# Kernel optimization log

Hardware: AMD Instinct MI355X
Metric: run time of the kernel (lower is better)

## Reference

```python
import jax, jax.numpy as jnp
import numpy as np

CLASS_EMBED_DIM = 128
TOPK = 64
EPS = float(np.finfo(float).eps)
ALPHA = 0.99


def setup_inputs() -> dict:
    key = jax.random.key(0)
    k1, k2, k3 = jax.random.split(key, 3)
    b, n, d = 16, 256, 640  # d = embed_dim + class_embed_dim
    embed_dim, inner_dim = 512, 512
    x = jax.random.normal(k1, (b, n, d), dtype=jnp.float32)
    # kaiming-normal style init: std = sqrt(2 / fan_in)
    std = (2.0 / embed_dim) ** 0.5
    Wq = jax.random.normal(k2, (embed_dim, inner_dim), dtype=jnp.float32) * std
    Wk = jax.random.normal(k3, (embed_dim, inner_dim), dtype=jnp.float32) * std
    alpha = jnp.float32(ALPHA)
    return {"x": x, "Wq": Wq, "Wk": Wk, "alpha": alpha}


def reference(x, Wq, Wk, alpha):
    b, n, d = x.shape
    xf = x.reshape(b * n, d)            # (N, embed+class)
    xe = xf[:, :-CLASS_EMBED_DIM]       # (N, embed)
    q = xe @ Wq                         # (N, inner)
    k = xe @ Wk                         # (N, inner)
    D = q.shape[1]
    # dots[i,j] = mean_d (q_i - k_j)^2, via expansion (avoids N x N x D tensor)
    q2 = jnp.sum(q * q, axis=1)
    k2 = jnp.sum(k * k, axis=1)
    dots = (q2[:, None] + k2[None, :] - 2.0 * (q @ k.T)) / D  # (N, N)
    N = dots.shape[0]
    _, idx = jax.lax.top_k(dots, TOPK)  # largest, matching torch.topk
    mask = jnp.zeros_like(dots).at[jnp.arange(N)[:, None], idx].set(1.0)
    mask = ((mask + mask.T) > 0).astype(jnp.float32)
    attn = dots * mask
    A = jnp.eye(N, dtype=dots.dtype) - alpha * attn + EPS
    out = jnp.linalg.inv(A) @ xf        # (N, d); to_v is identity
    return out.reshape(b, n, d)
```

## Files before the change

kernel.cpp:

```cpp
#include <hip/hip_runtime.h>
#include <float.h>

#define NN 4096
#define DD 640
#define DE 512
#define NB 16
#define OB 128
#define NOB (NN/OB)
#define SB 128
#define NSB (NN/SB)

static __device__ __forceinline__ float4 ldg4(const float* p) { return *(const float4*)p; }

__global__ __launch_bounds__(256) void proj_gemm(
    const float* __restrict__ xf, const float* __restrict__ Wq,
    const float* __restrict__ Wk, float* __restrict__ q, float* __restrict__ kk_)
{
  __shared__ float Xs[32][68], Qs[32][68], Ks[32][68];
  const int i0 = blockIdx.x * 64, c0 = blockIdx.y * 64;
  const int t = threadIdx.x, tr = t >> 4, tc = t & 15;
  float accq[4][4] = {}, acck[4][4] = {};
  for (int kb = 0; kb < DE; kb += 32) {
    {
      int m = t >> 3, k4 = (t & 7) << 2;
      float4 v0 = ldg4(xf + (size_t)(i0 + m) * DD + kb + k4);
      float4 v1 = ldg4(xf + (size_t)(i0 + m + 32) * DD + kb + k4);
      Xs[k4+0][m] = v0.x; Xs[k4+1][m] = v0.y; Xs[k4+2][m] = v0.z; Xs[k4+3][m] = v0.w;
      Xs[k4+0][m+32] = v1.x; Xs[k4+1][m+32] = v1.y; Xs[k4+2][m+32] = v1.z; Xs[k4+3][m+32] = v1.w;
    }
    {
      int kr = t >> 3, n8 = (t & 7) << 3;
      *(float4*)&Qs[kr][n8]   = ldg4(Wq + (size_t)(kb + kr) * DE + c0 + n8);
      *(float4*)&Qs[kr][n8+4] = ldg4(Wq + (size_t)(kb + kr) * DE + c0 + n8 + 4);
      *(float4*)&Ks[kr][n8]   = ldg4(Wk + (size_t)(kb + kr) * DE + c0 + n8);
      *(float4*)&Ks[kr][n8+4] = ldg4(Wk + (size_t)(kb + kr) * DE + c0 + n8 + 4);
    }
    __syncthreads();
    #pragma unroll
    for (int kkk = 0; kkk < 32; ++kkk) {
      float a[4], bq[4], bk[4];
      *(float4*)a  = *(const float4*)&Xs[kkk][tr << 2];
      *(float4*)bq = *(const float4*)&Qs[kkk][tc << 2];
      *(float4*)bk = *(const float4*)&Ks[kkk][tc << 2];
      #pragma unroll
      for (int r = 0; r < 4; ++r)
        #pragma unroll
        for (int c = 0; c < 4; ++c) { accq[r][c] += a[r]*bq[c]; acck[r][c] += a[r]*bk[c]; }
    }
    __syncthreads();
  }
  #pragma unroll
  for (int r = 0; r < 4; ++r) {
    float* qp = q   + (size_t)(i0 + (tr<<2) + r) * DE + c0 + (tc<<2);
    float* kp = kk_ + (size_t)(i0 + (tr<<2) + r) * DE + c0 + (tc<<2);
    *(float4*)qp = make_float4(accq[r][0], accq[r][1], accq[r][2], accq[r][3]);
    *(float4*)kp = make_float4(acck[r][0], acck[r][1], acck[r][2], acck[r][3]);
  }
}

__global__ __launch_bounds__(256) void rownorm(
    const float* __restrict__ q, const float* __restrict__ kk_,
    float* __restrict__ q2, float* __restrict__ k2)
{
  int w = (blockIdx.x * 256 + threadIdx.x) >> 6;
  int lane = threadIdx.x & 63;
  const float* src = (w < NN) ? q : kk_;
  int row = (w < NN) ? w : w - NN;
  const float* p = src + (size_t)row * DE;
  float s = 0.f;
  for (int c = lane; c < DE; c += 64) { float v = p[c]; s += v * v; }
  for (int off = 32; off; off >>= 1) s += __shfl_down(s, off);
  if (lane == 0) { if (w < NN) q2[row] = s; else k2[row] = s; }
}

__global__ __launch_bounds__(256) void dots_gemm(
    const float* __restrict__ q, const float* __restrict__ kk_,
    const float* __restrict__ q2, const float* __restrict__ k2,
    float* __restrict__ dots)
{
  __shared__ float Qs[32][68], Ks[32][68];
  const int i0 = blockIdx.x * 64, j0 = blockIdx.y * 64;
  const int t = threadIdx.x, tr = t >> 4, tc = t & 15;
  float acc[4][4] = {};
  for (int kb = 0; kb < DE; kb += 32) {
    int m = t >> 3, k4 = (t & 7) << 2;
    {
      float4 v0 = ldg4(q + (size_t)(i0 + m) * DE + kb + k4);
      float4 v1 = ldg4(q + (size_t)(i0 + m + 32) * DE + kb + k4);
      Qs[k4+0][m] = v0.x; Qs[k4+1][m] = v0.y; Qs[k4+2][m] = v0.z; Qs[k4+3][m] = v0.w;
      Qs[k4+0][m+32] = v1.x; Qs[k4+1][m+32] = v1.y; Qs[k4+2][m+32] = v1.z; Qs[k4+3][m+32] = v1.w;
    }
    {
      float4 v0 = ldg4(kk_ + (size_t)(j0 + m) * DE + kb + k4);
      float4 v1 = ldg4(kk_ + (size_t)(j0 + m + 32) * DE + kb + k4);
      Ks[k4+0][m] = v0.x; Ks[k4+1][m] = v0.y; Ks[k4+2][m] = v0.z; Ks[k4+3][m] = v0.w;
      Ks[k4+0][m+32] = v1.x; Ks[k4+1][m+32] = v1.y; Ks[k4+2][m+32] = v1.z; Ks[k4+3][m+32] = v1.w;
    }
    __syncthreads();
    #pragma unroll
    for (int kkk = 0; kkk < 32; ++kkk) {
      float a[4], b[4];
      *(float4*)a = *(const float4*)&Qs[kkk][tr << 2];
      *(float4*)b = *(const float4*)&Ks[kkk][tc << 2];
      #pragma unroll
      for (int r = 0; r < 4; ++r)
        #pragma unroll
        for (int c = 0; c < 4; ++c) acc[r][c] += a[r]*b[c];
    }
    __syncthreads();
  }
  const float inv = 1.0f / (float)DE;
  float k2v[4]; *(float4*)k2v = ldg4(k2 + j0 + (tc<<2));
  #pragma unroll
  for (int r = 0; r < 4; ++r) {
    float q2v = q2[i0 + (tr<<2) + r];
    float o[4];
    #pragma unroll
    for (int c = 0; c < 4; ++c) o[c] = (q2v + k2v[c] - 2.0f*acc[r][c]) * inv;
    *(float4*)(dots + (size_t)(i0 + (tr<<2) + r) * NN + j0 + (tc<<2)) =
        make_float4(o[0], o[1], o[2], o[3]);
  }
}

__global__ __launch_bounds__(256) void topk_bits(
    const float* __restrict__ dots, unsigned int* __restrict__ bits)
{
  __shared__ float row[NN];
  __shared__ unsigned int b[128];
  __shared__ float rv[4]; __shared__ int ri[4];
  const int i = blockIdx.x, t = threadIdx.x;
  const float* dr = dots + (size_t)i * NN;
  for (int c = t; c < NN; c += 256) row[c] = dr[c];
  if (t < 128) b[t] = 0u;
  __syncthreads();
  for (int it = 0; it < 64; ++it) {
    float bv = -FLT_MAX; int bi = NN;
    for (int c = t; c < NN; c += 256) { float v = row[c]; if (v > bv) { bv = v; bi = c; } }
    for (int off = 32; off; off >>= 1) {
      float ov = __shfl_down(bv, off); int oi = __shfl_down(bi, off);
      if (ov > bv || (ov == bv && oi < bi)) { bv = ov; bi = oi; }
    }
    if ((t & 63) == 0) { rv[t >> 6] = bv; ri[t >> 6] = bi; }
    __syncthreads();
    if (t == 0) {
      float fv = rv[0]; int fi = ri[0];
      for (int w = 1; w < 4; ++w)
        if (rv[w] > fv || (rv[w] == fv && ri[w] < fi)) { fv = rv[w]; fi = ri[w]; }
      b[fi >> 5] |= 1u << (fi & 31);
      row[fi] = -FLT_MAX;
    }
    __syncthreads();
  }
  if (t < 128) bits[(size_t)i * 128 + t] = b[t];
}

__global__ __launch_bounds__(256) void build_A(
    float* __restrict__ A, const unsigned int* __restrict__ bits,
    const float* __restrict__ alpha_p)
{
  int tid = blockIdx.x * 256 + threadIdx.x;
  int i = tid >> 10;
  int j4 = (tid & 1023) << 2;
  float alpha = alpha_p[0];
  float* p = A + (size_t)i * NN + j4;
  float4 d = *(float4*)p;
  unsigned int wrow = bits[(size_t)i * 128 + (j4 >> 5)];
  float dv[4] = {d.x, d.y, d.z, d.w}, o[4];
  #pragma unroll
  for (int u = 0; u < 4; ++u) {
    int j = j4 + u;
    unsigned int m1 = (wrow >> (j & 31)) & 1u;
    unsigned int m2 = (bits[(size_t)j * 128 + (i >> 5)] >> (i & 31)) & 1u;
    float base = (i == j) ? 1.0f : 0.0f;
    o[u] = base - ((m1 | m2) ? alpha * dv[u] : 0.0f);
  }
  *(float4*)p = make_float4(o[0], o[1], o[2], o[3]);
}

__global__ __launch_bounds__(1024) void lu_panel(
    float* __restrict__ A, int k0, int ok0, int* __restrict__ piv)
{
  const int t = threadIdx.x;
  const int M = NN - k0;
  float a[4][NB];
  __shared__ float bufA[NB], bufB[NB];
  __shared__ float rv[16]; __shared__ int ri[16];
  __shared__ int s_pr;
  __shared__ int piv_s[NB];
  __shared__ int sd[32], ss[32];
  __shared__ float l16[16][17];
  __shared__ float gbuf[32][112];

  #pragma unroll
  for (int i = 0; i < 4; ++i) {
    int r = t + (i << 10);
    if (r < M) {
      const float* src = A + (size_t)(k0 + r) * NN + k0;
      #pragma unroll
      for (int c4 = 0; c4 < NB; c4 += 4) {
        float4 v = ldg4(src + c4);
        a[i][c4] = v.x; a[i][c4+1] = v.y; a[i][c4+2] = v.z; a[i][c4+3] = v.w;
      }
    }
  }

  #pragma unroll
  for (int j = 0; j < NB; ++j) {
    float bv = -1.0f; int br = 1 << 30;
    #pragma unroll
    for (int i = 0; i < 4; ++i) {
      int r = t + (i << 10);
      if (r >= j && r < M) {
        float v = fabsf(a[i][j]);
        if (v > bv || (v == bv && r < br)) { bv = v; br = r; }
      }
    }
    for (int off = 32; off; off >>= 1) {
      float ov = __shfl_down(bv, off); int orr = __shfl_down(br, off);
      if (ov > bv || (ov == bv && orr < br)) { bv = ov; br = orr; }
    }
    if ((t & 63) == 0) { rv[t >> 6] = bv; ri[t >> 6] = br; }
    __syncthreads();
    if (t == 0) {
      float fv = rv[0]; int fr = ri[0];
      for (int w = 1; w < 16; ++w)
        if (rv[w] > fv || (rv[w] == fv && ri[w] < fr)) { fv = rv[w]; fr = ri[w]; }
      s_pr = fr; piv_s[j] = k0 + fr;
    }
    __syncthreads();
    const int pr = s_pr, prT = pr & 1023, prS = pr >> 10;
    if (t == prT) {
      #pragma unroll
      for (int i2 = 0; i2 < 4; ++i2) if (i2 == prS) {
        #pragma unroll
        for (int c = 0; c < NB; ++c) bufB[c] = a[i2][c];
      }
    }
    if (t == j) {
      #pragma unroll
      for (int c = 0; c < NB; ++c) bufA[c] = a[0][c];
    }
    __syncthreads();
    if (t == j) {
      #pragma unroll
      for (int c = 0; c < NB; ++c) a[0][c] = bufB[c];
    }
    if (t == prT) {
      #pragma unroll
      for (int i2 = 0; i2 < 4; ++i2) if (i2 == prS) {
        #pragma unroll
        for (int c = 0; c < NB; ++c) a[i2][c] = bufA[c];
      }
    }
    float rp = 1.0f / bufB[j];
    #pragma unroll
    for (int i = 0; i < 4; ++i) {
      int r = t + (i << 10);
      if (r > j && r < M) {
        float mlt = a[i][j] * rp;
        a[i][j] = mlt;
        #pragma unroll
        for (int c = j + 1; c < NB; ++c) a[i][c] -= mlt * bufB[c];
      }
    }
    __syncthreads();
  }

  #pragma unroll
  for (int i = 0; i < 4; ++i) {
    int r = t + (i << 10);
    if (r < M) {
      float* dst = A + (size_t)(k0 + r) * NN + k0;
      #pragma unroll
      for (int c4 = 0; c4 < NB; c4 += 4)
        *(float4*)(dst + c4) = make_float4(a[i][c4], a[i][c4+1], a[i][c4+2], a[i][c4+3]);
    }
  }
  if (t < NB) piv[k0 + t] = piv_s[t];

  if (t < 16) {
    #pragma unroll
    for (int c2 = 0; c2 < NB; ++c2) l16[t][c2] = a[0][c2];
  }

  if (t < 32) {
    int slotrow = (t < NB) ? (k0 + t) : -1;
    int content = slotrow;
    int next_ext = NB;
    for (int j = 0; j < NB; ++j) {
      int p = piv_s[j];
      unsigned long long mask = __ballot(slotrow == p);
      int bslot;
      if (mask) bslot = __ffsll((unsigned long long)mask) - 1;
      else {
        bslot = next_ext;
        if (t == next_ext) { slotrow = p; content = p; }
        next_ext++;
      }
      int srcl = (t == j) ? bslot : ((t == bslot) ? j : t);
      content = __shfl(content, srcl);
    }
    sd[t] = slotrow;
    ss[t] = content;
  }
  __syncthreads();

  const int p16 = k0 - ok0;
  for (int idx = t; idx < 32 * 112; idx += 1024) {
    int i = idx / 112, cc = idx - i * 112;
    if (sd[i] >= 0 && sd[i] != ss[i]) {
      int c = ok0 + (cc < p16 ? cc : cc + NB);
      gbuf[i][cc] = A[(size_t)ss[i] * NN + c];
    }
  }
  __syncthreads();
  for (int idx = t; idx < 32 * 112; idx += 1024) {
    int i = idx / 112, cc = idx - i * 112;
    if (sd[i] >= 0 && sd[i] != ss[i]) {
      int c = ok0 + (cc < p16 ? cc : cc + NB);
      A[(size_t)sd[i] * NN + c] = gbuf[i][cc];
    }
  }
  __syncthreads();

  const int w = ok0 + OB - (k0 + NB);
  if (t < w) {
    int c = k0 + NB + t;
    int cc = p16 + t;
    float x[16];
    #pragma unroll
    for (int i = 0; i < 16; ++i)
      x[i] = (ss[i] != sd[i]) ? gbuf[i][cc] : A[(size_t)(k0 + i) * NN + c];
    #pragma unroll
    for (int i = 1; i < 16; ++i)
      #pragma unroll
      for (int j = 0; j < i; ++j) x[i] -= l16[i][j] * x[j];
    #pragma unroll
    for (int i = 0; i < 16; ++i) A[(size_t)(k0 + i) * NN + c] = x[i];
  }
}

__global__ __launch_bounds__(128) void net_perm128(
    const int* __restrict__ piv_g, int ok0,
    int* __restrict__ nd, int* __restrict__ ns)
{
  __shared__ int slotrow[256], content[256];
  __shared__ int found, next_ext;
  const int t = threadIdx.x;
  slotrow[t] = ok0 + t;       content[t] = ok0 + t;
  slotrow[t + 128] = -1;      content[t + 128] = -1;
  if (t == 0) next_ext = 128;
  for (int j = 0; j < OB; ++j) {
    __syncthreads();
    int p = piv_g[ok0 + j];
    if (t == 0) found = (p < ok0 + OB) ? (p - ok0) : -1;
    __syncthreads();
    if (p >= ok0 + OB && slotrow[t + 128] == p) found = t + 128;
    __syncthreads();
    if (t == 0) {
      int s2 = found;
      if (s2 < 0) { s2 = next_ext++; slotrow[s2] = p; content[s2] = p; }
      int tmp = content[j]; content[j] = content[s2]; content[s2] = tmp;
    }
  }
  __syncthreads();
  nd[t] = slotrow[t];           ns[t] = content[t];
  nd[t + 128] = slotrow[t + 128]; ns[t + 128] = content[t + 128];
}

__global__ __launch_bounds__(256) void perm_copy_out(
    const float* __restrict__ A, float* __restrict__ T,
    const int* __restrict__ nd, const int* __restrict__ ns, int ok0)
{
  int s = blockIdx.y;
  int d = nd[s], sr = ns[s];
  if (d < 0 || d == sr) return;
  int c = blockIdx.x * 1024 + threadIdx.x * 4;
  if (c >= ok0 && c < ok0 + OB) return;
  *(float4*)(T + (size_t)s * NN + c) = ldg4(A + (size_t)sr * NN + c);
}

__global__ __launch_bounds__(256) void perm_copy_in(
    float* __restrict__ A, const float* __restrict__ T,
    const int* __restrict__ nd, const int* __restrict__ ns, int ok0)
{
  int s = blockIdx.y;
  int d = nd[s], sr = ns[s];
  if (d < 0 || d == sr) return;
  int c = blockIdx.x * 1024 + threadIdx.x * 4;
  if (c >= ok0 && c < ok0 + OB) return;
  *(float4*)(A + (size_t)d * NN + c) = ldg4(T + (size_t)s * NN + c);
}

__global__ __launch_bounds__(64) void trsm128L(float* __restrict__ A, int ok0)
{
  __shared__ float Ls[64][65];
  __shared__ float xs[64][132];
  const int t = threadIdx.x;
  const int c = ok0 + OB + blockIdx.x * 64 + t;
  for (int i = 0; i < 128; ++i) xs[t][i] = A[(size_t)(ok0 + i) * NN + c];
  for (int i = 0; i < 64; ++i) Ls[i][t] = A[(size_t)(ok0 + i) * NN + ok0 + t];
  __syncthreads();
  for (int i = 1; i < 64; ++i) {
    float s = 0.f;
    #pragma unroll 4
    for (int j = 0; j < i; ++j) s += Ls[i][j] * xs[t][j];
    xs[t][i] -= s;
  }
  __syncthreads();
  for (int i = 0; i < 64; ++i) Ls[i][t] = A[(size_t)(ok0 + 64 + i) * NN + ok0 + t];
  __syncthreads();
  for (int i = 0; i < 64; ++i) {
    float s = 0.f;
    #pragma unroll 4
    for (int j = 0; j < 64; ++j) s += Ls[i][j] * xs[t][j];
    xs[t][64 + i] -= s;
  }
  __syncthreads();
  for (int i = 0; i < 64; ++i) Ls[i][t] = A[(size_t)(ok0 + 64 + i) * NN + ok0 + 64 + t];
  __syncthreads();
  for (int i = 1; i < 64; ++i) {
    float s = 0.f;
    #pragma unroll 4
    for (int j = 0; j < i; ++j) s += Ls[i][j] * xs[t][64 + j];
    xs[t][64 + i] -= s;
  }
  for (int i = 0; i < 128; ++i) A[(size_t)(ok0 + i) * NN + c] = xs[t][i];
}

__global__ __launch_bounds__(256) void rank_update(
    float* __restrict__ C, int ldc,
    const float* __restrict__ Aop, int lda,
    const float* __restrict__ Bop, int ldb,
    int Mr, int Nc, int K)
{
  __shared__ float As[16][68], Bs[16][68];
  const int m0 = blockIdx.x * 64, n0 = blockIdx.y * 64;
  const int t = threadIdx.x, tr = t >> 4, tc = t & 15;
  const float4 z4 = make_float4(0.f, 0.f, 0.f, 0.f);
  float acc[4][4] = {};
  for (int kb = 0; kb < K; kb += 16) {
    {
      int m = t >> 2, k4 = (t & 3) << 2;
      float4 v0 = (m0 + m < Mr) ? ldg4(Aop + (size_t)(m0 + m) * lda + kb + k4) : z4;
      As[k4+0][m] = v0.x; As[k4+1][m] = v0.y; As[k4+2][m] = v0.z; As[k4+3][m] = v0.w;
    }
    {
      int kr = t >> 4, n4 = (t & 15) << 2;
      bool ok = (n0 + n4 < Nc);
      float4 w0 = ok ? ldg4(Bop + (size_t)(kb + kr) * ldb + n0 + n4) : z4;
      *(float4*)&Bs[kr][n4] = w0;
    }
    __syncthreads();
    #pragma unroll
    for (int kkk = 0; kkk < 16; ++kkk) {
      float a[4], b[4];
      *(float4*)a = *(const float4*)&As[kkk][tr << 2];
      *(float4*)b = *(const float4*)&Bs[kkk][tc << 2];
      #pragma unroll
      for (int r = 0; r < 4; ++r)
        #pragma unroll
        for (int c = 0; c < 4; ++c) acc[r][c] += a[r] * b[c];
    }
    __syncthreads();
  }
  #pragma unroll
  for (int r = 0; r < 4; ++r) {
    int m = m0 + (tr << 2) + r;
    int n = n0 + (tc << 2);
    if (m < Mr && n < Nc) {
      float* cp = C + (size_t)m * ldc + n;
      float4 cv = *(float4*)cp;
      cv.x -= acc[r][0]; cv.y -= acc[r][1]; cv.z -= acc[r][2]; cv.w -= acc[r][3];
      *(float4*)cp = cv;
    }
  }
}

__global__ __launch_bounds__(128) void inv_tri(
    const float* __restrict__ Ag, float* __restrict__ invT, int upper)
{
  __shared__ float xs[128][128];
  const int s = blockIdx.x, t = threadIdx.x;
  const size_t r0 = (size_t)s * SB;
  for (int i = 0; i < 128; ++i) xs[i][t] = 0.0f;
  const float* Tb = Ag + r0 * NN + r0;
  if (!upper) {
    xs[t][t] = 1.0f;
    for (int i = 1; i < 128; ++i) {
      float ssum = 0.f;
      for (int j = 0; j < i; ++j) ssum += Tb[(size_t)i * NN + j] * xs[j][t];
      if (i != t) xs[i][t] = -ssum;
    }
  } else {
    xs[t][t] = 1.0f / Tb[(size_t)t * NN + t];
    for (int i = 126; i >= 0; --i) {
      float ssum = 0.f;
      for (int j = i + 1; j < 128; ++j) ssum += Tb[(size_t)i * NN + j] * xs[j][t];
      if (i != t) xs[i][t] = -ssum / Tb[(size_t)i * NN + i];
    }
  }
  for (int i = 0; i < 128; ++i) invT[(size_t)s * SB * SB + (size_t)i * SB + t] = xs[i][t];
}

__global__ __launch_bounds__(1024) void perm_compose(
    const int* __restrict__ piv, int* __restrict__ idxp)
{
  __shared__ int pl[NN];
  const int t = threadIdx.x;
  for (int j = t; j < NN; j += 1024) pl[j] = piv[j];
  __syncthreads();
  int pos[4] = { t, t + 1024, t + 2048, t + 3072 };
  for (int j = NN - 1; j >= 0; --j) {
    int p = pl[j];
    #pragma unroll
    for (int u = 0; u < 4; ++u) {
      int r = t + (u << 10);
      if (j <= r) {
        if (pos[u] == j) pos[u] = p;
        else if (pos[u] == p) pos[u] = j;
      }
    }
  }
  #pragma unroll
  for (int u = 0; u < 4; ++u) idxp[t + (u << 10)] = pos[u];
}

__global__ __launch_bounds__(256) void gather_rows(
    const float* __restrict__ xf, const int* __restrict__ idxp, float* __restrict__ out)
{
  const int r = blockIdx.x, t = threadIdx.x;
  const int src = idxp[r];
  const float4* s = (const float4*)(xf + (size_t)src * DD);
  float4* d = (float4*)(out + (size_t)r * DD);
  for (int c = t; c < DD / 4; c += 256) d[c] = s[c];
}

__global__ __launch_bounds__(256) void diag_apply(
    float* __restrict__ B, const float* __restrict__ Minv, int r0)
{
  __shared__ float Bs[128][68];
  const int c0 = blockIdx.x * 64, t = threadIdx.x;
  #pragma unroll
  for (int v = 0; v < 8; ++v) {
    int id = t + v * 256;
    int k = id >> 4, c4 = (id & 15) << 2;
    *(float4*)&Bs[k][c4] = ldg4(B + (size_t)(r0 + k) * DD + c0 + c4);
  }
  __syncthreads();
  const int tr = t >> 4, tc = t & 15;
  float acc[8][4] = {};
  for (int k4 = 0; k4 < 128; k4 += 4) {
    float b0[4], b1[4], b2[4], b3[4];
    *(float4*)b0 = *(const float4*)&Bs[k4+0][tc << 2];
    *(float4*)b1 = *(const float4*)&Bs[k4+1][tc << 2];
    *(float4*)b2 = *(const float4*)&Bs[k4+2][tc << 2];
    *(float4*)b3 = *(const float4*)&Bs[k4+3][tc << 2];
    #pragma unroll
    for (int rr = 0; rr < 8; ++rr) {
      float m[4]; *(float4*)m = ldg4(Minv + (size_t)(tr*8 + rr) * SB + k4);
      #pragma unroll
      for (int c = 0; c < 4; ++c)
        acc[rr][c] += m[0]*b0[c] + m[1]*b1[c] + m[2]*b2[c] + m[3]*b3[c];
    }
  }
  #pragma unroll
  for (int rr = 0; rr < 8; ++rr)
    *(float4*)(B + (size_t)(r0 + tr*8 + rr) * DD + c0 + (tc << 2)) =
        make_float4(acc[rr][0], acc[rr][1], acc[rr][2], acc[rr][3]);
}

extern "C" void kernel_launch(void* const* d_in, const int* in_sizes, int n_in,
                              void* d_out, int out_size, void* d_ws, size_t ws_size,
                              hipStream_t stream)
{
  const float* xf    = (const float*)d_in[0];
  const float* Wq    = (const float*)d_in[1];
  const float* Wk    = (const float*)d_in[2];
  const float* alpha = (const float*)d_in[3];
  float* out = (float*)d_out;
  char* ws = (char*)d_ws;

  float* Amat = (float*)(ws);
  float* q    = (float*)(ws + 67108864ull);
  float* kbuf = (float*)(ws + 75497472ull);
  float* invL = (float*)(ws + 83886080ull);
  float* invU = (float*)(ws + 85983232ull);
  unsigned int* bits = (unsigned int*)(ws + 88080384ull);
  float* q2   = (float*)(ws + 90177536ull);
  float* k2   = (float*)(ws + 90193920ull);
  int* piv    = (int*)(ws + 90210304ull);
  int* idxp   = (int*)(ws + 90226688ull);
  int* nd     = (int*)(ws + 90243072ull);
  int* ns     = (int*)(ws + 90275840ull);
  float* Tbuf = q;

  proj_gemm<<<dim3(NN/64, DE/64), 256, 0, stream>>>(xf, Wq, Wk, q, kbuf);
  rownorm<<<2 * NN / 4, 256, 0, stream>>>(q, kbuf, q2, k2);
  dots_gemm<<<dim3(NN/64, NN/64), 256, 0, stream>>>(q, kbuf, q2, k2, Amat);
  topk_bits<<<NN, 256, 0, stream>>>(Amat, bits);
  build_A<<<NN * NN / 4 / 256, 256, 0, stream>>>(Amat, bits, alpha);

  for (int ob = 0; ob < NOB; ++ob) {
    const int ok0 = ob * OB;
    for (int p = 0; p < OB / NB; ++p) {
      const int k0 = ok0 + p * NB;
      lu_panel<<<1, 1024, 0, stream>>>(Amat, k0, ok0, piv);
      if (p < OB / NB - 1) {
        const int k1 = k0 + NB;
        const int w = ok0 + OB - k1;
        const int M2 = NN - k1;
        rank_update<<<dim3((M2 + 63) / 64, (w + 63) / 64), 256, 0, stream>>>(
            Amat + (size_t)k1 * NN + k1, NN,
            Amat + (size_t)k1 * NN + k0, NN,
            Amat + (size_t)k0 * NN + k1, NN,
            M2, w, NB);
      }
    }
    net_perm128<<<1, 128, 0, stream>>>(piv, ok0, nd, ns);
    perm_copy_out<<<dim3(NN / 1024, 256), 256, 0, stream>>>(Amat, Tbuf, nd, ns, ok0);
    perm_copy_in<<<dim3(NN / 1024, 256), 256, 0, stream>>>(Amat, Tbuf, nd, ns, ok0);
    const int b1 = ok0 + OB;
    const int M2 = NN - b1;
    if (M2 > 0) {
      trsm128L<<<M2 / 64, 64, 0, stream>>>(Amat, ok0);
      rank_update<<<dim3(M2 / 64, M2 / 64), 256, 0, stream>>>(
          Amat + (size_t)b1 * NN + b1, NN,
          Amat + (size_t)b1 * NN + ok0, NN,
          Amat + (size_t)ok0 * NN + b1, NN,
          M2, M2, OB);
    }
  }

  inv_tri<<<NSB, 128, 0, stream>>>(Amat, invL, 0);
  inv_tri<<<NSB, 128, 0, stream>>>(Amat, invU, 1);
  perm_compose<<<1, 1024, 0, stream>>>(piv, idxp);
  gather_rows<<<NN, 256, 0, stream>>>(xf, idxp, out);

  for (int s = 0; s < NSB; ++s) {
    int r0 = s * SB;
    diag_apply<<<DD / 64, 256, 0, stream>>>(out, invL + (size_t)s * SB * SB, r0);
    if (r0 + SB < NN) {
      int M2 = NN - r0 - SB;
      rank_update<<<dim3(M2 / 64, DD / 64), 256, 0, stream>>>(
          out + (size_t)(r0 + SB) * DD, DD,
          Amat + (size_t)(r0 + SB) * NN + r0, NN,
          out + (size_t)r0 * DD, DD,
          M2, DD, SB);
    }
  }
  for (int s = NSB - 1; s >= 0; --s) {
    int r0 = s * SB;
    diag_apply<<<DD / 64, 256, 0, stream>>>(out, invU + (size_t)s * SB * SB, r0);
    if (r0 > 0) {
      rank_update<<<dim3(r0 / 64, DD / 64), 256, 0, stream>>>(
          out, DD,
          Amat + r0, NN,
          out + (size_t)r0 * DD, DD,
          r0, DD, SB);
    }
  }
}
```

Measured before the change: 40.80 ms.

## Use 128x128 register-tiled trailing update, warp-level pivot permutation, split accumulators

Adds a rank_update128 kernel with 8x8 per-thread register tiles over 128x128 output tiles. It replaces the 64x64 kernel for the big trailing LU update and for both block triangular solves, raising arithmetic intensity. net_perm128 is rewritten as a single-wavefront kernel that uses ballot and shuffle instead of shared memory and repeated barriers. The trsm and triangular-inverse dot loops get four independent accumulators to break the FMA dependency chain, which also changes summation order slightly. The larger tiles mean fewer blocks on the small late-stage updates, and DD/128=5 assumes exact divisibility.

```diff
diff --git a/kernel.cpp b/kernel.cpp
--- a/kernel.cpp
+++ b/kernel.cpp
@@ -340,32 +340,50 @@
   }
 }
 
-__global__ __launch_bounds__(128) void net_perm128(
+__global__ __launch_bounds__(64) void net_perm128(
     const int* __restrict__ piv_g, int ok0,
     int* __restrict__ nd, int* __restrict__ ns)
 {
-  __shared__ int slotrow[256], content[256];
-  __shared__ int found, next_ext;
-  const int t = threadIdx.x;
-  slotrow[t] = ok0 + t;       content[t] = ok0 + t;
-  slotrow[t + 128] = -1;      content[t + 128] = -1;
-  if (t == 0) next_ext = 128;
+  __shared__ int pl[OB];
+  const int L = threadIdx.x;
+  pl[L] = piv_g[ok0 + L];
+  pl[L + 64] = piv_g[ok0 + 64 + L];
+  __syncthreads();
+  int c0 = ok0 + L, c1 = ok0 + 64 + L, c2 = -1, c3 = -1;
+  int sr2 = -1, sr3 = -1;
+  int next_ext = 128;
   for (int j = 0; j < OB; ++j) {
-    __syncthreads();
-    int p = piv_g[ok0 + j];
-    if (t == 0) found = (p < ok0 + OB) ? (p - ok0) : -1;
-    __syncthreads();
-    if (p >= ok0 + OB && slotrow[t + 128] == p) found = t + 128;
-    __syncthreads();
-    if (t == 0) {
-      int s2 = found;
-      if (s2 < 0) { s2 = next_ext++; slotrow[s2] = p; content[s2] = p; }
-      int tmp = content[j]; content[j] = content[s2]; content[s2] = tmp;
-    }
-  }
-  __syncthreads();
-  nd[t] = slotrow[t];           ns[t] = content[t];
-  nd[t + 128] = slotrow[t + 128]; ns[t + 128] = content[t + 128];
+    int p = pl[j];
+    int s2;
+    if (p < ok0 + OB) s2 = p - ok0;
+    else {
+      unsigned long long m2 = __ballot(sr2 == p);
+      unsigned long long m3 = __ballot(sr3 == p);
+      if (m2) s2 = 128 + (__ffsll(m2) - 1);
+      else if (m3) s2 = 192 + (__ffsll(m3) - 1);
+      else {
+        s2 = next_ext;
+        if (s2 < 192) { if (L == s2 - 128) { sr2 = p; c2 = p; } }
+        else          { if (L == s2 - 192) { sr3 = p; c3 = p; } }
+        next_ext++;
+      }
+    }
+    int jp = j >> 6, jl = j & 63, sp = s2 >> 6, sl = s2 & 63;
+    int vj0 = __shfl(c0, jl), vj1 = __shfl(c1, jl);
+    int vj = (jp == 0) ? vj0 : vj1;
+    int vs0 = __shfl(c0, sl), vs1 = __shfl(c1, sl), vs2 = __shfl(c2, sl), vs3 = __shfl(c3, sl);
+    int vs = (sp == 0) ? vs0 : (sp == 1) ? vs1 : (sp == 2) ? vs2 : vs3;
+    if (jp == 0 && L == jl) c0 = vs;
+    if (jp == 1 && L == jl) c1 = vs;
+    if (sp == 0 && L == sl) c0 = vj;
+    if (sp == 1 && L == sl) c1 = vj;
+    if (sp == 2 && L == sl) c2 = vj;
+    if (sp == 3 && L == sl) c3 = vj;
+  }
+  nd[L] = ok0 + L;        ns[L] = c0;
+  nd[64 + L] = ok0 + 64 + L; ns[64 + L] = c1;
+  nd[128 + L] = sr2;      ns[128 + L] = c2;
+  nd[192 + L] = sr3;      ns[192 + L] = c3;
 }
 
 __global__ __launch_bounds__(256) void perm_copy_out(
@@ -395,35 +413,46 @@
 __global__ __launch_bounds__(64) void trsm128L(float* __restrict__ A, int ok0)
 {
   __shared__ float Ls[64][65];
-  __shared__ float xs[64][132];
+  __shared__ float xs[64][133];
   const int t = threadIdx.x;
   const int c = ok0 + OB + blockIdx.x * 64 + t;
   for (int i = 0; i < 128; ++i) xs[t][i] = A[(size_t)(ok0 + i) * NN + c];
   for (int i = 0; i < 64; ++i) Ls[i][t] = A[(size_t)(ok0 + i) * NN + ok0 + t];
   __syncthreads();
   for (int i = 1; i < 64; ++i) {
-    float s = 0.f;
+    float s0 = 0.f, s1 = 0.f, s2 = 0.f, s3 = 0.f;
+    int j = 0;
+    for (; j + 3 < i; j += 4) {
+      s0 += Ls[i][j+0] * xs[t][j+0]; s1 += Ls[i][j+1] * xs[t][j+1];
+      s2 += Ls[i][j+2] * xs[t][j+2]; s3 += Ls[i][j+3] * xs[t][j+3];
+    }
+    for (; j < i; ++j) s0 += Ls[i][j] * xs[t][j];
+    xs[t][i] -= (s0 + s1) + (s2 + s3);
+  }
+  __syncthreads();
+  for (int i = 0; i < 64; ++i) Ls[i][t] = A[(size_t)(ok0 + 64 + i) * NN + ok0 + t];
+  __syncthreads();
+  for (int i = 0; i < 64; ++i) {
+    float s0 = 0.f, s1 = 0.f, s2 = 0.f, s3 = 0.f;
     #pragma unroll 4
-    for (int j = 0; j < i; ++j) s += Ls[i][j] * xs[t][j];
-    xs[t][i] -= s;
-  }
-  __syncthreads();
-  for (int i = 0; i < 64; ++i) Ls[i][t] = A[(size_t)(ok0 + 64 + i) * NN + ok0 + t];
-  __syncthreads();
-  for (int i = 0; i < 64; ++i) {
-    float s = 0.f;
-    #pragma unroll 4
-    for (int j = 0; j < 64; ++j) s += Ls[i][j] * xs[t][j];
-    xs[t][64 + i] -= s;
+    for (int j = 0; j < 64; j += 4) {
+      s0 += Ls[i][j+0] * xs[t][j+0]; s1 += Ls[i][j+1] * xs[t][j+1];
+      s2 += Ls[i][j+2] * xs[t][j+2]; s3 += Ls[i][j+3] * xs[t][j+3];
+    }
+    xs[t][64 + i] -= (s0 + s1) + (s2 + s3);
   }
   __syncthreads();
   for (int i = 0; i < 64; ++i) Ls[i][t] = A[(size_t)(ok0 + 64 + i) * NN + ok0 + 64 + t];
   __syncthreads();
   for (int i = 1; i < 64; ++i) {
-    float s = 0.f;
-    #pragma unroll 4
-    for (int j = 0; j < i; ++j) s += Ls[i][j] * xs[t][64 + j];
-    xs[t][64 + i] -= s;
+    float s0 = 0.f, s1 = 0.f, s2 = 0.f, s3 = 0.f;
+    int j = 0;
+    for (; j + 3 < i; j += 4) {
+      s0 += Ls[i][j+0] * xs[t][64+j+0]; s1 += Ls[i][j+1] * xs[t][64+j+1];
+      s2 += Ls[i][j+2] * xs[t][64+j+2]; s3 += Ls[i][j+3] * xs[t][64+j+3];
+    }
+    for (; j < i; ++j) s0 += Ls[i][j] * xs[t][64+j];
+    xs[t][64 + i] -= (s0 + s1) + (s2 + s3);
   }
   for (int i = 0; i < 128; ++i) A[(size_t)(ok0 + i) * NN + c] = xs[t][i];
 }
@@ -477,6 +506,56 @@
   }
 }
 
+__global__ __launch_bounds__(256) void rank_update128(
+    float* __restrict__ C, int ldc,
+    const float* __restrict__ Aop, int lda,
+    const float* __restrict__ Bop, int ldb,
+    int K)
+{
+  __shared__ float As[16][132], Bs[16][132];
+  const int m0 = blockIdx.x * 128, n0 = blockIdx.y * 128;
+  const int t = threadIdx.x;
+  const int tr = t >> 4, tc = t & 15;
+  float acc[8][8] = {};
+  for (int kb = 0; kb < K; kb += 16) {
+    {
+      int m = t >> 1, k8 = (t & 1) << 3;
+      const float* ap = Aop + (size_t)(m0 + m) * lda + kb + k8;
+      float4 v0 = ldg4(ap), v1 = ldg4(ap + 4);
+      As[k8+0][m] = v0.x; As[k8+1][m] = v0.y; As[k8+2][m] = v0.z; As[k8+3][m] = v0.w;
+      As[k8+4][m] = v1.x; As[k8+5][m] = v1.y; As[k8+6][m] = v1.z; As[k8+7][m] = v1.w;
+    }
+    {
+      int kr = t >> 4, c8 = (t & 15) << 3;
+      const float* bp = Bop + (size_t)(kb + kr) * ldb + n0 + c8;
+      *(float4*)&Bs[kr][c8]     = ldg4(bp);
+      *(float4*)&Bs[kr][c8 + 4] = ldg4(bp + 4);
+    }
+    __syncthreads();
+    #pragma unroll
+    for (int k = 0; k < 16; ++k) {
+      float av[8], bv[8];
+      *(float4*)av       = *(const float4*)&As[k][tr << 3];
+      *(float4*)(av + 4) = *(const float4*)&As[k][(tr << 3) + 4];
+      *(float4*)bv       = *(const float4*)&Bs[k][tc << 3];
+      *(float4*)(bv + 4) = *(const float4*)&Bs[k][(tc << 3) + 4];
+      #pragma unroll
+      for (int r = 0; r < 8; ++r)
+        #pragma unroll
+        for (int c = 0; c < 8; ++c) acc[r][c] += av[r] * bv[c];
+    }
+    __syncthreads();
+  }
+  #pragma unroll
+  for (int r = 0; r < 8; ++r) {
+    float* cp = C + (size_t)(m0 + (tr << 3) + r) * ldc + n0 + (tc << 3);
+    float4 c0 = *(float4*)cp, c1 = *(float4*)(cp + 4);
+    c0.x -= acc[r][0]; c0.y -= acc[r][1]; c0.z -= acc[r][2]; c0.w -= acc[r][3];
+    c1.x -= acc[r][4]; c1.y -= acc[r][5]; c1.z -= acc[r][6]; c1.w -= acc[r][7];
+    *(float4*)cp = c0; *(float4*)(cp + 4) = c1;
+  }
+}
+
 __global__ __launch_bounds__(128) void inv_tri(
     const float* __restrict__ Ag, float* __restrict__ invT, int upper)
 {
@@ -488,15 +567,31 @@
   if (!upper) {
     xs[t][t] = 1.0f;
     for (int i = 1; i < 128; ++i) {
-      float ssum = 0.f;
-      for (int j = 0; j < i; ++j) ssum += Tb[(size_t)i * NN + j] * xs[j][t];
+      float s0 = 0.f, s1 = 0.f, s2 = 0.f, s3 = 0.f;
+      int j = 0;
+      for (; j + 3 < i; j += 4) {
+        s0 += Tb[(size_t)i * NN + j+0] * xs[j+0][t];
+        s1 += Tb[(size_t)i * NN + j+1] * xs[j+1][t];
+        s2 += Tb[(size_t)i * NN + j+2] * xs[j+2][t];
+        s3 += Tb[(size_t)i * NN + j+3] * xs[j+3][t];
+      }
+      for (; j < i; ++j) s0 += Tb[(size_t)i * NN + j] * xs[j][t];
+      float ssum = (s0 + s1) + (s2 + s3);
       if (i != t) xs[i][t] = -ssum;
     }
   } else {
     xs[t][t] = 1.0f / Tb[(size_t)t * NN + t];
     for (int i = 126; i >= 0; --i) {
-      float ssum = 0.f;
-      for (int j = i + 1; j < 128; ++j) ssum += Tb[(size_t)i * NN + j] * xs[j][t];
+      float s0 = 0.f, s1 = 0.f, s2 = 0.f, s3 = 0.f;
+      int j = i + 1;
+      for (; j + 3 < 128; j += 4) {
+        s0 += Tb[(size_t)i * NN + j+0] * xs[j+0][t];
+        s1 += Tb[(size_t)i * NN + j+1] * xs[j+1][t];
+        s2 += Tb[(size_t)i * NN + j+2] * xs[j+2][t];
+        s3 += Tb[(size_t)i * NN + j+3] * xs[j+3][t];
+      }
+      for (; j < 128; ++j) s0 += Tb[(size_t)i * NN + j] * xs[j][t];
+      float ssum = (s0 + s1) + (s2 + s3);
       if (i != t) xs[i][t] = -ssum / Tb[(size_t)i * NN + i];
     }
   }
@@ -617,18 +712,18 @@
             M2, w, NB);
       }
     }
-    net_perm128<<<1, 128, 0, stream>>>(piv, ok0, nd, ns);
+    net_perm128<<<1, 64, 0, stream>>>(piv, ok0, nd, ns);
     perm_copy_out<<<dim3(NN / 1024, 256), 256, 0, stream>>>(Amat, Tbuf, nd, ns, ok0);
     perm_copy_in<<<dim3(NN / 1024, 256), 256, 0, stream>>>(Amat, Tbuf, nd, ns, ok0);
     const int b1 = ok0 + OB;
     const int M2 = NN - b1;
     if (M2 > 0) {
       trsm128L<<<M2 / 64, 64, 0, stream>>>(Amat, ok0);
-      rank_update<<<dim3(M2 / 64, M2 / 64), 256, 0, stream>>>(
+      rank_update128<<<dim3(M2 / 128, M2 / 128), 256, 0, stream>>>(
           Amat + (size_t)b1 * NN + b1, NN,
           Amat + (size_t)b1 * NN + ok0, NN,
           Amat + (size_t)ok0 * NN + b1, NN,
-          M2, M2, OB);
+          OB);
     }
   }
 
@@ -642,22 +737,22 @@
     diag_apply<<<DD / 64, 256, 0, stream>>>(out, invL + (size_t)s * SB * SB, r0);
     if (r0 + SB < NN) {
       int M2 = NN - r0 - SB;
-      rank_update<<<dim3(M2 / 64, DD / 64), 256, 0, stream>>>(
+      rank_update128<<<dim3(M2 / 128, DD / 128), 256, 0, stream>>>(
           out + (size_t)(r0 + SB) * DD, DD,
           Amat + (size_t)(r0 + SB) * NN + r0, NN,
           out + (size_t)r0 * DD, DD,
-          M2, DD, SB);
+          SB);
     }
   }
   for (int s = NSB - 1; s >= 0; --s) {
     int r0 = s * SB;
     diag_apply<<<DD / 64, 256, 0, stream>>>(out, invU + (size_t)s * SB * SB, r0);
     if (r0 > 0) {
-      rank_update<<<dim3(r0 / 64, DD / 64), 256, 0, stream>>>(
+      rank_update128<<<dim3(r0 / 128, DD / 128), 256, 0, stream>>>(
           out, DD,
           Amat + r0, NN,
           out + (size_t)r0 * DD, DD,
-          r0, DD, SB);
-    }
-  }
-}
+          SB);
+    }
+  }
+}
```

Result: no change. 41.26 ms (+1.1%).
